# Performance work log

Measured on AMD Instinct MI355X. Metric: run time of the kernel, lower is better.

The kernel has to match this reference:

```python
import jax, jax.numpy as jnp
import numpy as np

T_Q, T_K, B, H, V = 32, 48, 64, 1024, 32320
MASK_FILL = -65504.0  # GNMT uses fp16 min


def setup_inputs() -> dict:
    key = jax.random.key(0)
    ks = jax.random.split(key, 12)
    s = 0.02
    inp = {
        "input1": jax.random.normal(ks[0], (T_K, B, H), jnp.float32),
        "input0": jax.random.normal(ks[1], (T_K, B, H), jnp.float32),
        "input2": jax.random.randint(ks[2], (B,), 1, T_K + 1),          # context lengths in [1, T_K]
        "input3": jax.random.randint(ks[3], (T_Q, B), 0, V),            # decoder token ids
        "emb": (jax.random.normal(ks[4], (V, H), jnp.float32) * 0.1).at[0].set(0.0),  # padding_idx=0
        "W_ih": jax.random.normal(ks[5], (4 * H, H), jnp.float32) * s,
        "W_hh": jax.random.normal(ks[6], (4 * H, H), jnp.float32) * s,
        "b_ih": jnp.zeros((4 * H,), jnp.float32),
        "b_hh": jnp.zeros((4 * H,), jnp.float32),
        "W_q": jax.random.normal(ks[7], (H, H), jnp.float32) * s,
        "W_k": jax.random.normal(ks[8], (H, H), jnp.float32) * s,
        "v_att": jax.random.normal(ks[9], (H,), jnp.float32) * s,
        "norm_scalar": jnp.array([1.0 / np.sqrt(H)], jnp.float32),
        "norm_bias": jnp.zeros((H,), jnp.float32),
    }
    return inp


def _lstm(x, W_ih, W_hh, b_ih, b_hh):
    # x: (T, B, In). PyTorch LSTM gate order: i, f, g, o. Zero initial state.
    xp = jnp.einsum('tbi,gi->tbg', x, W_ih) + b_ih + b_hh  # (T, B, 4H)
    Hh = W_hh.shape[1]

    def step(carry, xt):
        h, c = carry
        gates = xt + h @ W_hh.T
        i, f, g, o = jnp.split(gates, 4, axis=-1)
        c = jax.nn.sigmoid(f) * c + jax.nn.sigmoid(i) * jnp.tanh(g)
        h = jax.nn.sigmoid(o) * jnp.tanh(c)
        return (h, c), h

    h0 = jnp.zeros((x.shape[1], Hh), x.dtype)
    _, hs = jax.lax.scan(step, (h0, h0), xp)
    return hs  # (T, B, H)


def _forward(input1, input0, input2, input3, emb, W_ih, W_hh, b_ih, b_hh,
             W_q, W_k, v_att, norm_scalar, norm_bias):
    x = emb[input3]                       # (T_Q, B, H) embedding lookup
    ctx = input0 + input1                 # (T_K, B, H) residual-summed encoder context
    rnn_out = _lstm(x, W_ih, W_hh, b_ih, b_hh)   # (T_Q, B, H)

    # Bahdanau attention (batch_first=False -> transpose to batch-first)
    q = rnn_out.transpose(1, 0, 2)        # (B, T_Q, H)
    keys = ctx.transpose(1, 0, 2)         # (B, T_K, H)
    aq = q @ W_q.T                        # (B, T_Q, H)
    ak = keys @ W_k.T                     # (B, T_K, H)
    v = v_att / jnp.linalg.norm(v_att) * norm_scalar[0]  # normalized attention vector
    sum_qk = aq[:, :, None, :] + ak[:, None, :, :] + norm_bias  # (B, T_Q, T_K, H)
    scores = jnp.einsum('bqkh,h->bqk', jnp.tanh(sum_qk), v)
    pad = jnp.arange(T_K)[None, :] >= input2[:, None]            # (B, T_K), True = pad
    scores = jnp.where(pad[:, None, :], MASK_FILL, scores)
    attn = jax.nn.softmax(scores, axis=-1)
    context = jnp.einsum('bqk,bkh->bqh', attn, keys).transpose(1, 0, 2)  # (T_Q, B, H)
    # dropout p=0 -> identity; returns (rnn_outputs, attn_context) = (out12, out11)
    return rnn_out, context


def reference(input1, input0, input2, input3, emb, W_ih, W_hh, b_ih, b_hh,
              W_q, W_k, v_att, norm_scalar, norm_bias):
    return _forward(input1, input0, input2, input3, emb, W_ih, W_hh, b_ih, b_hh,
                    W_q, W_k, v_att, norm_scalar, norm_bias)
```

## Files before the change

kernel.cpp:

```cpp
#include <hip/hip_runtime.h>
#include <hip/hip_bf16.h>

typedef unsigned short u16;
typedef __attribute__((ext_vector_type(8))) short bf16x8;
typedef __attribute__((ext_vector_type(8))) unsigned short us8;
typedef __attribute__((ext_vector_type(4))) float f32x4;

#define T_Q 32
#define T_K 48
#define NB 64
#define HDIM 1024
#define MASK_FILL -65504.0f
#define LSTM_BLOCKS 64

__device__ __forceinline__ float bf2f(u16 v){
  union { unsigned u; float f; } x; x.u = ((unsigned)v) << 16; return x.f;
}
__device__ __forceinline__ u16 f2bf(float f){
  union { float f; unsigned u; } x; x.f = f;
  return (u16)((x.u + 0x7FFFu + ((x.u >> 16) & 1u)) >> 16);
}
__device__ __forceinline__ float sigm(float x){
  return __builtin_amdgcn_rcpf(1.f + __expf(-x));
}
__device__ __forceinline__ float tanh_f(float x){
  float e = __expf(2.f * x);
  return fmaf(-2.f, __builtin_amdgcn_rcpf(e + 1.f), 1.f);
}

__device__ __forceinline__ void st_b32_cc(u16* a, unsigned v){
  asm volatile("global_store_dword %0, %1, off sc0 sc1" :: "v"(a), "v"(v) : "memory");
}
__device__ __forceinline__ void st_flag(int* a, int v){
  asm volatile("global_store_dword %0, %1, off sc0 sc1" :: "v"(a), "v"(v) : "memory");
}
__device__ __forceinline__ int ld_flag(const int* a){
  int r;
  asm volatile("global_load_dword %0, %1, off sc0 sc1\n\ts_waitcnt vmcnt(0)"
               : "=v"(r) : "v"(a) : "memory");
  return r;
}

#define MFMA16(A,B,C) __builtin_amdgcn_mfma_f32_16x16x32_bf16(A,B,C,0,0,0)


__global__ void conv_f2b(const float* __restrict__ s, u16* __restrict__ d){
  size_t i = ((size_t)blockIdx.x * 256 + threadIdx.x) * 4;
  float4 v = *(const float4*)(s + i);
  ushort4 o; o.x = f2bf(v.x); o.y = f2bf(v.y); o.z = f2bf(v.z); o.w = f2bf(v.w);
  *(ushort4*)(d + i) = o;
}

__global__ void gather_x(const int* __restrict__ tok, const float* __restrict__ emb,
                         u16* __restrict__ x){
  int r = blockIdx.x;
  int token = tok[r];
  float4 v = ((const float4*)(emb + (size_t)token * HDIM))[threadIdx.x];
  ushort4 o; o.x = f2bf(v.x); o.y = f2bf(v.y); o.z = f2bf(v.z); o.w = f2bf(v.w);
  ((ushort4*)(x + (size_t)r * HDIM))[threadIdx.x] = o;
}

__global__ void make_keys(const float* __restrict__ a, const float* __restrict__ b,
                          u16* __restrict__ o){
  size_t i = ((size_t)blockIdx.x * 256 + threadIdx.x) * 4;
  float4 va = *(const float4*)(a + i);
  float4 vb = *(const float4*)(b + i);
  ushort4 vo;
  vo.x = f2bf(va.x + vb.x);
  vo.y = f2bf(va.y + vb.y);
  vo.z = f2bf(va.z + vb.z);
  vo.w = f2bf(va.w + vb.w);
  *(ushort4*)(o + i) = vo;
}

__global__ void prep_small(const float* __restrict__ vatt, const float* __restrict__ ns,
                           const float* __restrict__ nb,
                           float* __restrict__ vhat, float* __restrict__ nbias){
  __shared__ float wred[4];
  int t = threadIdx.x, lane = t & 63, w = t >> 6;
  float vv[4]; float s = 0.f;
  #pragma unroll
  for (int j = 0; j < 4; j++){ vv[j] = vatt[t*4 + j]; s += vv[j]*vv[j]; }
  #pragma unroll
  for (int m = 32; m >= 1; m >>= 1) s += __shfl_xor(s, m);
  if (lane == 0) wred[w] = s;
  __syncthreads();
  float tot = wred[0] + wred[1] + wred[2] + wred[3];
  float scale = ns[0] / sqrtf(tot);
  #pragma unroll
  for (int j = 0; j < 4; j++) vhat[t*4 + j] = vv[j] * scale;
  #pragma unroll
  for (int j = 0; j < 4; j++){ int i = t + 256*j; nbias[i] = nb[i]; }
}

__global__ void prep_bsum(const float* __restrict__ bih, const float* __restrict__ bhh,
                          float* __restrict__ bias_sum){
  int i = blockIdx.x * 256 + threadIdx.x;
  bias_sum[i] = bih[i] + bhh[i];
}


template<int OB>
__global__ __launch_bounds__(256) void gemm128(
  const u16* __restrict__ A, const u16* __restrict__ W,
  const float* __restrict__ bias, void* __restrict__ Cv,
  int M, int N, int K)
{
  __shared__ __align__(16) u16 As[128][32];
  __shared__ __align__(16) u16 Bs[128][32];
  const int t = threadIdx.x;
  const int m0 = blockIdx.y * 128, n0 = blockIdx.x * 128;
  const int lane = t & 63, w = t >> 6;
  const int wm = (w >> 1) * 64, wn = (w & 1) * 64;
  const int lr = lane & 15, g = lane >> 4;
  const int srow = t >> 2, skc = t & 3;

  f32x4 acc[4][4];
  #pragma unroll
  for (int i = 0; i < 4; i++)
    #pragma unroll
    for (int j = 0; j < 4; j++) acc[i][j] = (f32x4){0,0,0,0};

  const u16* aptr0 = A + (size_t)(m0 + srow)      * K + skc * 8;
  const u16* aptr1 = A + (size_t)(m0 + 64 + srow) * K + skc * 8;
  const u16* wptr0 = W + (size_t)(n0 + srow)      * K + skc * 8;
  const u16* wptr1 = W + (size_t)(n0 + 64 + srow) * K + skc * 8;

  for (int k0 = 0; k0 < K; k0 += 32){
    bf16x8 va0 = *(const bf16x8*)(aptr0 + k0);
    bf16x8 va1 = *(const bf16x8*)(aptr1 + k0);
    bf16x8 vb0 = *(const bf16x8*)(wptr0 + k0);
    bf16x8 vb1 = *(const bf16x8*)(wptr1 + k0);
    *(bf16x8*)(&As[srow][skc * 8])      = va0;
    *(bf16x8*)(&As[64 + srow][skc * 8]) = va1;
    *(bf16x8*)(&Bs[srow][skc * 8])      = vb0;
    *(bf16x8*)(&Bs[64 + srow][skc * 8]) = vb1;
    __syncthreads();
    bf16x8 af[4], bfr[4];
    #pragma unroll
    for (int mi = 0; mi < 4; mi++) af[mi]  = *(const bf16x8*)(&As[wm + mi * 16 + lr][g * 8]);
    #pragma unroll
    for (int ni = 0; ni < 4; ni++) bfr[ni] = *(const bf16x8*)(&Bs[wn + ni * 16 + lr][g * 8]);
    #pragma unroll
    for (int mi = 0; mi < 4; mi++)
      #pragma unroll
      for (int ni = 0; ni < 4; ni++)
        acc[mi][ni] = MFMA16(af[mi], bfr[ni], acc[mi][ni]);
    __syncthreads();
  }

  float bv[4];
  #pragma unroll
  for (int ni = 0; ni < 4; ni++) bv[ni] = bias ? bias[n0 + wn + ni * 16 + lr] : 0.f;
  #pragma unroll
  for (int mi = 0; mi < 4; mi++){
    #pragma unroll
    for (int r = 0; r < 4; r++){
      const size_t row = (size_t)(m0 + wm + mi * 16 + g * 4 + r);
      #pragma unroll
      for (int ni = 0; ni < 4; ni++){
        float v = acc[mi][ni][r] + bv[ni];
        const size_t col = (size_t)(n0 + wn + ni * 16 + lr);
        if (OB) ((u16*)Cv)[row * N + col] = f2bf(v);
        else    ((float*)Cv)[row * N + col] = v;
      }
    }
  }
}


__global__ __launch_bounds__(512, 1) void lstm_persistent(
  const float* __restrict__ Whh, const u16* __restrict__ xp,
  u16* __restrict__ hsteps,
  u16* __restrict__ qbuf, float* __restrict__ out0,
  int* __restrict__ flags)
{
  extern __shared__ char smem[];
  u16*  wlds = (u16*)smem;
  float* gl  = (float*)(smem + 131072);

  const int tid = threadIdx.x;
  const int c0 = blockIdx.x * 16;
  const int lane = tid & 63, w = tid >> 6;
  const int gate = w & 3, msub = w >> 2;
  const int lr = lane & 15, g = lane >> 4;

  #pragma unroll
  for (int i = 0; i < 16; i++){
    int e = (i * 512 + tid) * 8;
    int R = e >> 10, k = e & 1023;
    int gg = R >> 4, rr = R & 15, tt = k >> 5, kk = k & 31;
    const float* src = Whh + (size_t)((gg << 10) + c0 + rr) * 1024 + k;
    float4 v0 = *(const float4*)(src);
    float4 v1 = *(const float4*)(src + 4);
    u16* dst = wlds + (((gg * 32 + tt) * 16 + rr) * 32 + kk);
    ushort4 o0, o1;
    o0.x = f2bf(v0.x); o0.y = f2bf(v0.y); o0.z = f2bf(v0.z); o0.w = f2bf(v0.w);
    o1.x = f2bf(v1.x); o1.y = f2bf(v1.y); o1.z = f2bf(v1.z); o1.w = f2bf(v1.w);
    *(ushort4*)dst = o0; *(ushort4*)(dst + 4) = o1;
  }
  __syncthreads();

  const int pb = (tid * 2) >> 4;
  const int pc = (tid * 2) & 15;
  float c_state0 = 0.f, c_state1 = 0.f;

  const int arow = msub * 32 + lr;
  const int jc = g >> 1;
  const int cc = (g & 1) * 8;

  #pragma unroll 1
  for (int step = 0; step < T_Q; step++){
    const u16* xr = xp + ((size_t)(step * NB + pb)) * 4096 + c0 + pc;
    unsigned xw0 = *(const unsigned*)(xr);
    unsigned xw1 = *(const unsigned*)(xr + 1024);
    unsigned xw2 = *(const unsigned*)(xr + 2048);
    unsigned xw3 = *(const unsigned*)(xr + 3072);

    f32x4 acc0 = {0,0,0,0}, acc1 = {0,0,0,0};

    if (step > 0){
      if (w == 0){
        const int* fp = flags + lane * 16;
        for (;;){
          int f = ld_flag(fp);
          if (__ballot(f >= step) == ~0ull) break;
          __builtin_amdgcn_s_sleep(1);
        }
      }
      __syncthreads();

      const u16* hb = hsteps + (size_t)(step - 1) * 65536;
      const u16* pa0 = hb + (size_t)jc * 1024 + (size_t)arow * 16 + cc;
      const u16* pa1 = pa0 + 256;
      bf16x8 a0[8], a1[8];
      #pragma unroll
      for (int p = 0; p < 8; p++){
        a0[p] = *(const bf16x8*)(pa0 + p * 2048);
        a1[p] = *(const bf16x8*)(pa1 + p * 2048);
      }
      #pragma unroll
      for (int t = 0; t < 32; t++){
        bf16x8 bfr = *(const bf16x8*)(wlds + ((size_t)(gate * 32 + t) * 16 + lr) * 32 + g * 8);
        acc0 = MFMA16(a0[t & 7], bfr, acc0);
        acc1 = MFMA16(a1[t & 7], bfr, acc1);
        if (t < 24){
          a0[t & 7] = *(const bf16x8*)(pa0 + (t + 8) * 2048);
          a1[t & 7] = *(const bf16x8*)(pa1 + (t + 8) * 2048);
        }
      }
    }

    #pragma unroll
    for (int r = 0; r < 4; r++){
      gl[(gate * 64 + msub * 32 +      g * 4 + r) * 16 + lr] = acc0[r];
      gl[(gate * 64 + msub * 32 + 16 + g * 4 + r) * 16 + lr] = acc1[r];
    }
    __syncthreads();

    float hout0, hout1; u16 hb0, hb1;
    {
      float ig = gl[(0 * 64 + pb) * 16 + pc] + bf2f((u16)(xw0 & 0xFFFF));
      float fg = gl[(1 * 64 + pb) * 16 + pc] + bf2f((u16)(xw1 & 0xFFFF));
      float gg = gl[(2 * 64 + pb) * 16 + pc] + bf2f((u16)(xw2 & 0xFFFF));
      float og = gl[(3 * 64 + pb) * 16 + pc] + bf2f((u16)(xw3 & 0xFFFF));
      float cn = sigm(fg) * c_state0 + sigm(ig) * tanh_f(gg);
      c_state0 = cn;
      hout0 = sigm(og) * tanh_f(cn); hb0 = f2bf(hout0);
    }
    {
      float ig = gl[(0 * 64 + pb) * 16 + pc + 1] + bf2f((u16)(xw0 >> 16));
      float fg = gl[(1 * 64 + pb) * 16 + pc + 1] + bf2f((u16)(xw1 >> 16));
      float gg = gl[(2 * 64 + pb) * 16 + pc + 1] + bf2f((u16)(xw2 >> 16));
      float og = gl[(3 * 64 + pb) * 16 + pc + 1] + bf2f((u16)(xw3 >> 16));
      float cn = sigm(fg) * c_state1 + sigm(ig) * tanh_f(gg);
      c_state1 = cn;
      hout1 = sigm(og) * tanh_f(cn); hb1 = f2bf(hout1);
    }

    if (step < T_Q - 1){
      u16* hw = hsteps + (size_t)step * 65536 + (size_t)blockIdx.x * 1024 + pb * 16 + pc;
      unsigned hpack = (unsigned)hb0 | ((unsigned)hb1 << 16);
      st_b32_cc(hw, hpack);
      asm volatile("s_waitcnt vmcnt(0)" ::: "memory");
      __syncthreads();
      if (tid == 0) st_flag(flags + blockIdx.x * 16, step + 1);
    }

    ushort2 hh; hh.x = hb0; hh.y = hb1;
    *(ushort2*)(qbuf + ((size_t)pb * T_Q + step) * HDIM + c0 + pc) = hh;
    float2 ho; ho.x = hout0; ho.y = hout1;
    *(float2*)(out0 + ((size_t)(step * NB + pb)) * HDIM + c0 + pc) = ho;
  }
}


__global__ __launch_bounds__(256) void attn_fused(
  const float* __restrict__ aq, const u16* __restrict__ ak,
  const float* __restrict__ vhat, const u16* __restrict__ keys,
  const int* __restrict__ lens, float* __restrict__ out1)
{
  int b = blockIdx.x >> 5, q = blockIdx.x & 31;
  int t = threadIdx.x, lane = t & 63, w = t >> 6;
  __shared__ float sc[T_K];
  __shared__ float ps[T_K];
  int len = lens[b];
  float aqr[16], vh[16];
  const float* aqp = aq + (size_t)(b * T_Q + q) * HDIM + lane * 16;
  const float* vp  = vhat + lane * 16;
  #pragma unroll
  for (int j = 0; j < 4; j++){
    float4 v0 = ((const float4*)aqp)[j];
    float4 v1 = ((const float4*)vp)[j];
    aqr[j*4+0] = v0.x; aqr[j*4+1] = v0.y; aqr[j*4+2] = v0.z; aqr[j*4+3] = v0.w;
    vh[j*4+0]  = v1.x; vh[j*4+1]  = v1.y; vh[j*4+2]  = v1.z; vh[j*4+3]  = v1.w;
  }

  int kmax = len - w * 12; if (kmax > 12) kmax = 12;
  for (int kk = 0; kk < kmax; kk++){
    int k = w * 12 + kk;
    const u16* akp = ak + (size_t)(k * NB + b) * HDIM + lane * 16;
    us8 a0 = *(const us8*)(akp);
    us8 a1 = *(const us8*)(akp + 8);
    float p = 0.f;
    #pragma unroll
    for (int j = 0; j < 8; j++){
      p += tanh_f(aqr[j]     + bf2f(a0[j])) * vh[j];
      p += tanh_f(aqr[8 + j] + bf2f(a1[j])) * vh[8 + j];
    }
    #pragma unroll
    for (int m = 32; m >= 1; m >>= 1) p += __shfl_xor(p, m);
    if (lane == 0) sc[k] = p;
  }
  __syncthreads();
  float mx = -3.0e38f;
  for (int k = 0; k < len; k++) mx = fmaxf(mx, sc[k]);
  if (t < len) ps[t] = __expf(sc[t] - mx);
  __syncthreads();
  float den = 0.f;
  for (int k = 0; k < len; k++) den += ps[k];
  float rden = __builtin_amdgcn_rcpf(den);

  float c0 = 0.f, c1 = 0.f, c2 = 0.f, c3 = 0.f;
  for (int k = 0; k < len; k++){
    float pk = ps[k];
    ushort4 kv = *(const ushort4*)(keys + (size_t)(k * NB + b) * HDIM + t * 4);
    c0 += pk * bf2f(kv.x); c1 += pk * bf2f(kv.y);
    c2 += pk * bf2f(kv.z); c3 += pk * bf2f(kv.w);
  }
  size_t o = (size_t)(q * NB + b) * HDIM + t * 4;
  out1[o + 0] = c0 * rden;
  out1[o + 1] = c1 * rden;
  out1[o + 2] = c2 * rden;
  out1[o + 3] = c3 * rden;
}


extern "C" void kernel_launch(void* const* d_in, const int* in_sizes, int n_in,
                              void* d_out, int out_size, void* d_ws, size_t ws_size,
                              hipStream_t stream)
{
  const float* in1  = (const float*)d_in[0];
  const float* in0  = (const float*)d_in[1];
  const int*   lens = (const int*)d_in[2];
  const int*   toks = (const int*)d_in[3];
  const float* emb  = (const float*)d_in[4];
  const float* Wih  = (const float*)d_in[5];
  const float* Whh  = (const float*)d_in[6];
  const float* bih  = (const float*)d_in[7];
  const float* bhh  = (const float*)d_in[8];
  const float* Wq   = (const float*)d_in[9];
  const float* Wk   = (const float*)d_in[10];
  const float* vatt = (const float*)d_in[11];
  const float* ns   = (const float*)d_in[12];
  const float* nbb  = (const float*)d_in[13];

  char* p = (char*)d_ws;
  u16* x_bf    = (u16*)p;   p += (size_t)2048 * 1024 * 2;
  u16* keys_bf = (u16*)p;   p += (size_t)3072 * 1024 * 2;
  u16* hsteps  = (u16*)p;   p += (size_t)32 * 65536 * 2;
  u16* qbuf    = (u16*)p;   p += (size_t)2048 * 1024 * 2;
  u16* xp      = (u16*)p;   p += (size_t)2048 * 4096 * 2;
  float* vhat  = (float*)p; p += 1024 * 4;
  float* bsum  = (float*)p; p += 4096 * 4;
  float* nbf   = (float*)p; p += 1024 * 4;
  int* flags   = (int*)p;   p += 4096;
  u16* ak      = (u16*)p;   p += (size_t)3072 * 1024 * 2;
  u16* Wih_bf  = (u16*)p;   p += (size_t)4096 * 1024 * 2;
  u16* Wq_bf   = (u16*)p;   p += (size_t)1024 * 1024 * 2;
  u16* Wk_bf   = (u16*)p;   p += (size_t)1024 * 1024 * 2;
  float* aq    = (float*)xp;

  float* out0 = (float*)d_out;
  float* out1 = out0 + (size_t)T_Q * NB * HDIM;

  hipMemsetAsync(flags, 0, 4096, stream);

  conv_f2b<<<4096, 256, 0, stream>>>(Wih, Wih_bf);
  conv_f2b<<<1024, 256, 0, stream>>>(Wq,  Wq_bf);
  conv_f2b<<<1024, 256, 0, stream>>>(Wk,  Wk_bf);
  gather_x<<<2048, 256, 0, stream>>>(toks, emb, x_bf);
  make_keys<<<3072, 256, 0, stream>>>(in1, in0, keys_bf);
  prep_small<<<1, 256, 0, stream>>>(vatt, ns, nbb, vhat, nbf);
  prep_bsum<<<16, 256, 0, stream>>>(bih, bhh, bsum);

  gemm128<1><<<dim3(32, 16), 256, 0, stream>>>(x_bf, Wih_bf, bsum, xp, 2048, 4096, 1024);
  gemm128<1><<<dim3(8, 24), 256, 0, stream>>>(keys_bf, Wk_bf, nbf, ak, 3072, 1024, 1024);

  lstm_persistent<<<LSTM_BLOCKS, 512, 147456, stream>>>(Whh, xp, hsteps, qbuf, out0, flags);

  gemm128<0><<<dim3(8, 16), 256, 0, stream>>>(qbuf, Wq_bf, nullptr, aq, 2048, 1024, 1024);

  attn_fused<<<2048, 256, 0, stream>>>(aq, ak, vhat, keys_bf, lens, out1);
}
```

Before: 347.4 us.

## Overlap LSTM hidden-state loads with per-group flag arrival; pad GEMM LDS tiles

The persistent LSTM kernel no longer waits for all 64 producer blocks before a block-wide barrier. Wave 0 now publishes per-group readiness (8 groups of 8 blocks) through LDS flags, and all waves spin on each group's flag. Each wave then loads and multiplies that slice of the previous hidden state while later groups are still arriving, using double-buffered register sets. Separately, the GEMM shared tiles are padded from 32 to 40 columns to reduce LDS bank conflicts. The LDS spin-waits add polling overhead and rely on volatile LDS ordering being correct.

```diff
diff --git a/kernel.cpp b/kernel.cpp
--- a/kernel.cpp
+++ b/kernel.cpp
@@ -106,8 +106,8 @@
   const float* __restrict__ bias, void* __restrict__ Cv,
   int M, int N, int K)
 {
-  __shared__ __align__(16) u16 As[128][32];
-  __shared__ __align__(16) u16 Bs[128][32];
+  __shared__ __align__(16) u16 As[128][40];
+  __shared__ __align__(16) u16 Bs[128][40];
   const int t = threadIdx.x;
   const int m0 = blockIdx.y * 128, n0 = blockIdx.x * 128;
   const int lane = t & 63, w = t >> 6;
@@ -178,12 +178,15 @@
   extern __shared__ char smem[];
   u16*  wlds = (u16*)smem;
   float* gl  = (float*)(smem + 131072);
+  volatile int* lds_ready = (volatile int*)(smem + 147456);
 
   const int tid = threadIdx.x;
   const int c0 = blockIdx.x * 16;
   const int lane = tid & 63, w = tid >> 6;
   const int gate = w & 3, msub = w >> 2;
   const int lr = lane & 15, g = lane >> 4;
+
+  if (tid < 8) lds_ready[tid] = 0;
 
   #pragma unroll
   for (int i = 0; i < 16; i++){
@@ -209,6 +212,28 @@
   const int jc = g >> 1;
   const int cc = (g & 1) * 8;
 
+#define SPING(gq) \
+  do { while (lds_ready[gq] < step) __builtin_amdgcn_s_sleep(1); \
+       asm volatile("" ::: "memory"); } while (0)
+
+#define LOADG(s0, s1, gq) \
+  do { const u16* A0_ = pa0 + (gq) * 8192; const u16* A1_ = pa1 + (gq) * 8192; \
+       s0[0] = *(const bf16x8*)(A0_);        s1[0] = *(const bf16x8*)(A1_); \
+       s0[1] = *(const bf16x8*)(A0_ + 2048); s1[1] = *(const bf16x8*)(A1_ + 2048); \
+       s0[2] = *(const bf16x8*)(A0_ + 4096); s1[2] = *(const bf16x8*)(A1_ + 4096); \
+       s0[3] = *(const bf16x8*)(A0_ + 6144); s1[3] = *(const bf16x8*)(A1_ + 6144); } while (0)
+
+#define MFMAG(s0, s1, gq) \
+  do { const u16* wb_ = wlds + ((size_t)(gate * 32 + (gq) * 4) * 16 + lr) * 32 + g * 8; \
+       bf16x8 b0_ = *(const bf16x8*)(wb_); \
+       bf16x8 b1_ = *(const bf16x8*)(wb_ + 512); \
+       bf16x8 b2_ = *(const bf16x8*)(wb_ + 1024); \
+       bf16x8 b3_ = *(const bf16x8*)(wb_ + 1536); \
+       acc0 = MFMA16(s0[0], b0_, acc0); acc1 = MFMA16(s1[0], b0_, acc1); \
+       acc0 = MFMA16(s0[1], b1_, acc0); acc1 = MFMA16(s1[1], b1_, acc1); \
+       acc0 = MFMA16(s0[2], b2_, acc0); acc1 = MFMA16(s1[2], b2_, acc1); \
+       acc0 = MFMA16(s0[3], b3_, acc0); acc1 = MFMA16(s1[3], b3_, acc1); } while (0)
+
   #pragma unroll 1
   for (int step = 0; step < T_Q; step++){
     const u16* xr = xp + ((size_t)(step * NB + pb)) * 4096 + c0 + pc;
@@ -221,34 +246,37 @@
 
     if (step > 0){
       if (w == 0){
+        unsigned done = 0;
         const int* fp = flags + lane * 16;
-        for (;;){
+        while (done != 0xFFu){
           int f = ld_flag(fp);
-          if (__ballot(f >= step) == ~0ull) break;
-          __builtin_amdgcn_s_sleep(1);
+          unsigned long long b = __ballot(f >= step);
+          #pragma unroll
+          for (int gq = 0; gq < 8; gq++){
+            if (((done >> gq) & 1u) == 0 &&
+                ((unsigned)(b >> (gq * 8)) & 0xFFu) == 0xFFu){
+              if (lane == 0) lds_ready[gq] = step;
+              done |= 1u << gq;
+            }
+          }
+          if (done != 0xFFu) __builtin_amdgcn_s_sleep(1);
         }
       }
-      __syncthreads();
-
-      const u16* hb = hsteps + (size_t)(step - 1) * 65536;
+
+      const u16* hb  = hsteps + (size_t)(step - 1) * 65536;
       const u16* pa0 = hb + (size_t)jc * 1024 + (size_t)arow * 16 + cc;
       const u16* pa1 = pa0 + 256;
-      bf16x8 a0[8], a1[8];
-      #pragma unroll
-      for (int p = 0; p < 8; p++){
-        a0[p] = *(const bf16x8*)(pa0 + p * 2048);
-        a1[p] = *(const bf16x8*)(pa1 + p * 2048);
-      }
-      #pragma unroll
-      for (int t = 0; t < 32; t++){
-        bf16x8 bfr = *(const bf16x8*)(wlds + ((size_t)(gate * 32 + t) * 16 + lr) * 32 + g * 8);
-        acc0 = MFMA16(a0[t & 7], bfr, acc0);
-        acc1 = MFMA16(a1[t & 7], bfr, acc1);
-        if (t < 24){
-          a0[t & 7] = *(const bf16x8*)(pa0 + (t + 8) * 2048);
-          a1[t & 7] = *(const bf16x8*)(pa1 + (t + 8) * 2048);
-        }
-      }
+
+      bf16x8 sA0[4], sA1[4], sB0[4], sB1[4];
+      SPING(0); LOADG(sA0, sA1, 0);
+      SPING(1); LOADG(sB0, sB1, 1); MFMAG(sA0, sA1, 0);
+      SPING(2); LOADG(sA0, sA1, 2); MFMAG(sB0, sB1, 1);
+      SPING(3); LOADG(sB0, sB1, 3); MFMAG(sA0, sA1, 2);
+      SPING(4); LOADG(sA0, sA1, 4); MFMAG(sB0, sB1, 3);
+      SPING(5); LOADG(sB0, sB1, 5); MFMAG(sA0, sA1, 4);
+      SPING(6); LOADG(sA0, sA1, 6); MFMAG(sB0, sB1, 5);
+      SPING(7); LOADG(sB0, sB1, 7); MFMAG(sA0, sA1, 6);
+      MFMAG(sB0, sB1, 7);
     }
 
     #pragma unroll
@@ -292,6 +320,9 @@
     float2 ho; ho.x = hout0; ho.y = hout1;
     *(float2*)(out0 + ((size_t)(step * NB + pb)) * HDIM + c0 + pc) = ho;
   }
+#undef SPING
+#undef LOADG
+#undef MFMAG
 }
 
 
@@ -407,7 +438,7 @@
   gemm128<1><<<dim3(32, 16), 256, 0, stream>>>(x_bf, Wih_bf, bsum, xp, 2048, 4096, 1024);
   gemm128<1><<<dim3(8, 24), 256, 0, stream>>>(keys_bf, Wk_bf, nbf, ak, 3072, 1024, 1024);
 
-  lstm_persistent<<<LSTM_BLOCKS, 512, 147456, stream>>>(Whh, xp, hsteps, qbuf, out0, flags);
+  lstm_persistent<<<LSTM_BLOCKS, 512, 147488, stream>>>(Whh, xp, hsteps, qbuf, out0, flags);
 
   gemm128<0><<<dim3(8, 16), 256, 0, stream>>>(qbuf, Wq_bf, nullptr, aq, 2048, 1024, 1024);
 
```

Measured after the change: 347.7 us. No clear change (+0.1%).
